# Kernel tuning notes

Hardware: AMD Instinct MI355X
Metric: run time of the kernel (lower is better)

The kernel has to match this reference:

```python
import jax, jax.numpy as jnp
import numpy as np
from jax import lax

B, T, IN, H, OUT = 64, 2048, 128, 256, 1


def setup_inputs() -> dict:
    key = jax.random.key(0)
    ks = jax.random.split(key, 11)
    s_in = 1.0 / np.sqrt(H)
    return {
        "x": jax.random.normal(ks[0], (B, T, IN), dtype=jnp.float32),
        "W_ih0": jax.random.normal(ks[1], (H, IN), dtype=jnp.float32) * s_in,
        "W_hh0": jax.random.normal(ks[2], (H, H), dtype=jnp.float32) * s_in,
        "b_ih0": jax.random.normal(ks[3], (H,), dtype=jnp.float32) * s_in,
        "b_hh0": jax.random.normal(ks[4], (H,), dtype=jnp.float32) * s_in,
        "W_ih1": jax.random.normal(ks[5], (H, H), dtype=jnp.float32) * s_in,
        "W_hh1": jax.random.normal(ks[6], (H, H), dtype=jnp.float32) * s_in,
        "b_ih1": jax.random.normal(ks[7], (H,), dtype=jnp.float32) * s_in,
        "b_hh1": jax.random.normal(ks[8], (H,), dtype=jnp.float32) * s_in,
        "W_fc": jax.random.normal(ks[9], (OUT, H), dtype=jnp.float32) * s_in,
        "b_fc": jax.random.normal(ks[10], (OUT,), dtype=jnp.float32) * s_in,
    }


def _rnn_layer(inp, W_ih, W_hh, b_ih, b_hh):
    # Precompute input projection for all timesteps in one big GEMM: [B,T,H]
    xp = jnp.einsum('bti,hi->bth', inp, W_ih) + b_ih + b_hh
    h0 = jnp.zeros((inp.shape[0], W_hh.shape[0]), dtype=inp.dtype)

    def step(h, xt):  # xt: [B,H]
        h_new = jnp.tanh(xt + h @ W_hh.T)
        return h_new, h_new

    _, hs = lax.scan(step, h0, jnp.swapaxes(xp, 0, 1))  # hs: [T,B,H]
    return jnp.swapaxes(hs, 0, 1)  # [B,T,H]


def reference(x, W_ih0, W_hh0, b_ih0, b_hh0, W_ih1, W_hh1, b_ih1, b_hh1, W_fc, b_fc):
    h1 = _rnn_layer(x, W_ih0, W_hh0, b_ih0, b_hh0)   # layer 0 (dropout_prob=0.0)
    h2 = _rnn_layer(h1, W_ih1, W_hh1, b_ih1, b_hh1)  # layer 1
    last = h2[:, -1, :]                              # [B,H]
    return last @ W_fc.T + b_fc                      # [B,OUT]
```

## Files before the change

### kernel.cpp

```cpp
#include <hip/hip_runtime.h>
#include <math.h>

constexpr int Bb  = 64;
constexpr int Tt  = 2048;
constexpr int INN = 128;
constexpr int HH  = 256;
constexpr int ROWS = Bb * Tt;
constexpr int CH  = 64;
constexpr int NCH = Tt / CH;
constexpr int PS  = HH + 4;

__device__ int g_flag0[Bb];
__device__ int g_flag1[Bb];
__device__ int g_flag1b[Bb];

__device__ __forceinline__ void wait_flag(int* flag, int want)
{
    while (__hip_atomic_load(flag, __ATOMIC_RELAXED,
                             __HIP_MEMORY_SCOPE_SYSTEM) < want)
        __builtin_amdgcn_s_sleep(8);
    __builtin_amdgcn_fence(__ATOMIC_ACQUIRE, "agent");
}

__device__ __forceinline__ void wait_flag2(int* fa, int* fb, int want)
{
    for (;;) {
        int a = __hip_atomic_load(fa, __ATOMIC_RELAXED, __HIP_MEMORY_SCOPE_SYSTEM);
        int c = __hip_atomic_load(fb, __ATOMIC_RELAXED, __HIP_MEMORY_SCOPE_SYSTEM);
        if (a >= want && c >= want) break;
        __builtin_amdgcn_s_sleep(8);
    }
    __builtin_amdgcn_fence(__ATOMIC_ACQUIRE, "agent");
}

__device__ __forceinline__ void release_flag(int* flag, int val)
{
    __hip_atomic_store(flag, val, __ATOMIC_RELEASE, __HIP_MEMORY_SCOPE_AGENT);
}

__device__ __forceinline__ void lds_barrier()
{
    asm volatile("s_waitcnt lgkmcnt(0)" ::: "memory");
    __builtin_amdgcn_s_barrier();
}

__global__ __launch_bounds__(256) void ih_gemm(const float* in, const float* W,
                                               const float* bias1, const float* bias2,
                                               float* out)
{
    __shared__ float a_lds[16][68];
    __shared__ float b_lds[16][260];

    const int tid = threadIdx.x;
    if (blockIdx.x == 0 && tid < Bb) {
        g_flag0[tid] = 0; g_flag1[tid] = 0; g_flag1b[tid] = 0;
    }

    const int tx  = tid & 31;
    const int ty  = tid >> 5;
    const int row0 = blockIdx.x * 64;

    float acc[8][8];
#pragma unroll
    for (int r = 0; r < 8; ++r)
#pragma unroll
        for (int c = 0; c < 8; ++c) acc[r][c] = 0.f;

    for (int k0 = 0; k0 < INN; k0 += 16) {
#pragma unroll
        for (int i = 0; i < 4; ++i) {
            int e = i * 256 + tid;
            int r = e >> 4, kk = e & 15;
            a_lds[kk][r] = in[(row0 + r) * INN + k0 + kk];
        }
#pragma unroll
        for (int i = 0; i < 16; ++i) {
            int e = i * 256 + tid;
            int j = e >> 4, kk = e & 15;
            b_lds[kk][j] = W[j * INN + k0 + kk];
        }
        __syncthreads();

#pragma unroll
        for (int kk = 0; kk < 16; ++kk) {
            float4 a0 = *(const float4*)&a_lds[kk][ty * 8];
            float4 a1 = *(const float4*)&a_lds[kk][ty * 8 + 4];
            float4 b0 = *(const float4*)&b_lds[kk][tx * 8];
            float4 b1 = *(const float4*)&b_lds[kk][tx * 8 + 4];
            float av[8] = {a0.x, a0.y, a0.z, a0.w, a1.x, a1.y, a1.z, a1.w};
            float bv[8] = {b0.x, b0.y, b0.z, b0.w, b1.x, b1.y, b1.z, b1.w};
#pragma unroll
            for (int r = 0; r < 8; ++r)
#pragma unroll
                for (int c = 0; c < 8; ++c)
                    acc[r][c] += av[r] * bv[c];
        }
        __syncthreads();
    }

    float bsum[8];
#pragma unroll
    for (int c = 0; c < 8; ++c) {
        int j = tx * 8 + c;
        bsum[c] = bias1[j] + bias2[j];
    }
#pragma unroll
    for (int r = 0; r < 8; ++r) {
        int row = row0 + ty * 8 + r;
        float4 o0 = make_float4(acc[r][0] + bsum[0], acc[r][1] + bsum[1],
                                acc[r][2] + bsum[2], acc[r][3] + bsum[3]);
        float4 o1 = make_float4(acc[r][4] + bsum[4], acc[r][5] + bsum[5],
                                acc[r][6] + bsum[6], acc[r][7] + bsum[7]);
        *(float4*)&out[row * HH + tx * 8]     = o0;
        *(float4*)&out[row * HH + tx * 8 + 4] = o1;
    }
}

__device__ __forceinline__ float fast_tanh(float x)
{
    float e = __builtin_amdgcn_exp2f(x * 2.8853900817779268f);
    return fmaf(-2.0f, __builtin_amdgcn_rcpf(e + 1.0f), 1.0f);
}

__device__ __forceinline__ float fold32(float s)
{
#if __has_builtin(__builtin_amdgcn_permlane32_swap)
    typedef unsigned uint2v __attribute__((ext_vector_type(2)));
    uint2v r = __builtin_amdgcn_permlane32_swap(__float_as_uint(s), __float_as_uint(s),
                                                false, false);
    return __uint_as_float(r[0]) + __uint_as_float(r[1]);
#else
    return s + __shfl_xor(s, 32, 64);
#endif
}

__device__ __forceinline__ void load_wreg(const float* W, int l, int w,
                                          float (&wreg)[4][32])
{
#pragma unroll
    for (int r = 0; r < 4; ++r) {
        const float4* wp = (const float4*)&W[(size_t)(4 * l + r) * HH + 32 * w];
#pragma unroll
        for (int q = 0; q < 8; ++q) {
            float4 v = wp[q];
            wreg[r][4 * q + 0] = v.x;
            wreg[r][4 * q + 1] = v.y;
            wreg[r][4 * q + 2] = v.z;
            wreg[r][4 * q + 3] = v.w;
        }
    }
}

__device__ __forceinline__ void mac_partials(float hv, const float (&wreg)[4][32],
                                             float* wr)
{
    float p0 = 0.f, p1 = 0.f, p2 = 0.f, p3 = 0.f;
#pragma unroll
    for (int c = 0; c < 32; ++c) {
        float hcv = __int_as_float(__builtin_amdgcn_readlane(__float_as_int(hv), c));
        p0 = fmaf(wreg[0][c], hcv, p0);
        p1 = fmaf(wreg[1][c], hcv, p1);
        p2 = fmaf(wreg[2][c], hcv, p2);
        p3 = fmaf(wreg[3][c], hcv, p3);
    }
    *(float4*)wr = make_float4(p0, p1, p2, p3);
}

template <bool FS>
__device__ __forceinline__ void rnn_step(const float* rd, float* wr,
                                         float*& pw, const float* pr,
                                         float& xg, const float (&wreg)[4][32],
                                         bool lane_lt32)
{
    float xg2 = *pr;

    float s0 = rd[0 * PS], s1 = rd[1 * PS], s2 = rd[2 * PS], s3 = rd[3 * PS];
    float s = (s0 + s1) + (s2 + s3);
    s = fold32(s);

    float hv = fast_tanh(s + xg);
    if (lane_lt32) *pw = hv;

    mac_partials(hv, wreg, wr);

    if (FS) __syncthreads(); else lds_barrier();
    xg = xg2;
    pw += HH;
}

template <bool PROD>
__device__ void rnn_role(float* xpb, const float* Whh, float* sh, int b)
{
    float* pbufA = sh;
    float* pbufB = sh + 8 * PS;

    const int tid = threadIdx.x;
    const int w   = tid >> 6;
    const int l   = tid & 63;
    const int hf  = l >> 5;
    const int jr  = 32 * w + (l & 31);
    const bool lane_lt32 = (l < 32);

    float wreg[4][32];
    load_wreg(Whh, l, w, wreg);

    const float* rdA = &pbufA[4 * hf * PS + jr];
    const float* rdB = &pbufB[4 * hf * PS + jr];
    float*       wrA = &pbufA[w * PS + 4 * l];
    float*       wrB = &pbufB[w * PS + 4 * l];

    *(float4*)wrA = make_float4(0.f, 0.f, 0.f, 0.f);
    float xg = PROD ? xpb[jr] : 0.f;
    float* pw = xpb + jr;
    const float* pr = xpb + HH + jr;
    __syncthreads();

#pragma unroll 1
    for (int c = 0; c < NCH; ++c) {
        if (!PROD) {
            wait_flag2(&g_flag1[b], &g_flag1b[b], (c + 1) * (CH / 2));
            xg = xpb[(size_t)c * CH * HH + jr];
        }
#pragma unroll 1
        for (int p = 0; p < CH / 2 - 1; ++p) {
            rnn_step<false>(rdA, wrB, pw, pr, xg, wreg, lane_lt32); pr += HH;
            rnn_step<false>(rdB, wrA, pw, pr, xg, wreg, lane_lt32); pr += HH;
        }
        if (c < NCH - 1) {
            rnn_step<false>(rdA, wrB, pw, pr, xg, wreg, lane_lt32); pr += HH;
            rnn_step<PROD>(rdB, wrA, pw, pr, xg, wreg, lane_lt32);  pr += HH;
        } else {
            rnn_step<false>(rdA, wrB, pw, pr, xg, wreg, lane_lt32);
            rnn_step<PROD>(rdB, wrA, pw, pr, xg, wreg, lane_lt32);
        }
        if (PROD && tid == 0)
            release_flag(&g_flag0[b], (c + 1) * CH);
    }
}

__device__ __forceinline__ void gemm_phase(const float* rd, float* wr,
                                           float*& pw, const float* pr,
                                           float& xg, const float (&wreg)[4][32],
                                           float bsc, bool lane_lt32)
{
    float xg2 = *pr;

    float s0 = rd[0 * PS], s1 = rd[1 * PS], s2 = rd[2 * PS], s3 = rd[3 * PS];
    float s = (s0 + s1) + (s2 + s3);
    s = fold32(s);
    if (lane_lt32) *pw = s + bsc;

    mac_partials(xg, wreg, wr);

    lds_barrier();
    xg = xg2;
    pw += HH;
}

__device__ void gemm_role(float* ws, const float* W,
                          const float* b1, const float* b2, float* sh,
                          int b, int half)
{
    float* pbufA = sh;
    float* pbufB = sh + 8 * PS;

    const int tid = threadIdx.x;
    const int w   = tid >> 6;
    const int l   = tid & 63;
    const int hf  = l >> 5;
    const int jr  = 32 * w + (l & 31);
    const bool lane_lt32 = (l < 32);

    float wreg[4][32];
    load_wreg(W, l, w, wreg);
    const float bsc = b1[jr] + b2[jr];

    const float* rdA = &pbufA[4 * hf * PS + jr];
    const float* rdB = &pbufB[4 * hf * PS + jr];
    float*       wrA = &pbufA[w * PS + 4 * l];
    float*       wrB = &pbufB[w * PS + 4 * l];

    int* myflag = half ? &g_flag1b[b] : &g_flag1[b];

#pragma unroll 1
    for (int c = 0; c < NCH; ++c) {
        wait_flag(&g_flag0[b], (c + 1) * CH);

        float* Ab = ws + ((size_t)b * Tt + (size_t)c * CH + 32 * half) * HH;

        float xg  = Ab[jr];
        float xg2 = Ab[HH + jr];
        mac_partials(xg, wreg, wrB);
        lds_barrier();
        xg = xg2;

        float* pw = Ab + jr;
        const float* pr = Ab + 2 * HH + jr;

#pragma unroll 1
        for (int p = 0; p < 15; ++p) {
            gemm_phase(rdB, wrA, pw, pr, xg, wreg, bsc, lane_lt32); pr += HH;
            gemm_phase(rdA, wrB, pw, pr, xg, wreg, bsc, lane_lt32); pr += HH;
        }
        gemm_phase(rdB, wrA, pw, pr - HH, xg, wreg, bsc, lane_lt32);

        {
            float s0 = rdA[0 * PS], s1 = rdA[1 * PS];
            float s2 = rdA[2 * PS], s3 = rdA[3 * PS];
            float s = (s0 + s1) + (s2 + s3);
            s = fold32(s);
            if (lane_lt32) *pw = s + bsc;
            __syncthreads();
        }

        if (tid == 0)
            release_flag(myflag, (c + 1) * (CH / 2));
    }
}

__global__ __launch_bounds__(512, 2) void pipeline_kernel(
        float* ws, const float* Whh0, const float* Wih1,
        const float* bih1, const float* bhh1, const float* Whh1)
{
    __shared__ __attribute__((aligned(16))) float sh[2 * 8 * PS];

    const int bid = blockIdx.x;

    if (bid < 64) {
        rnn_role<true>(ws + (size_t)bid * Tt * HH, Whh0, sh, bid);
    } else if (bid < 192) {
        const int pidx = bid - 64;
        gemm_role(ws, Wih1, bih1, bhh1, sh, pidx >> 1, pidx & 1);
    } else {
        const int b = bid - 192;
        rnn_role<false>(ws + (size_t)b * Tt * HH, Whh1, sh, b);
    }
}

__global__ __launch_bounds__(64) void fc_kernel(const float* h2, const float* Wfc,
                                                const float* bfc, float* out)
{
    const int b = blockIdx.x;
    const int l = threadIdx.x;
    const float* hrow = h2 + ((size_t)b * Tt + (Tt - 1)) * HH;
    float4 hv = *(const float4*)&hrow[4 * l];
    float4 wv = *(const float4*)&Wfc[4 * l];
    float p = hv.x * wv.x + hv.y * wv.y + hv.z * wv.z + hv.w * wv.w;
#pragma unroll
    for (int off = 32; off > 0; off >>= 1) p += __shfl_down(p, off, 64);
    if (l == 0) out[b] = p + bfc[0];
}

extern "C" void kernel_launch(void* const* d_in, const int* in_sizes, int n_in,
                              void* d_out, int out_size, void* d_ws, size_t ws_size,
                              hipStream_t stream)
{
    const float* x     = (const float*)d_in[0];
    const float* W_ih0 = (const float*)d_in[1];
    const float* W_hh0 = (const float*)d_in[2];
    const float* b_ih0 = (const float*)d_in[3];
    const float* b_hh0 = (const float*)d_in[4];
    const float* W_ih1 = (const float*)d_in[5];
    const float* W_hh1 = (const float*)d_in[6];
    const float* b_ih1 = (const float*)d_in[7];
    const float* b_hh1 = (const float*)d_in[8];
    const float* W_fc  = (const float*)d_in[9];
    const float* b_fc  = (const float*)d_in[10];
    float* ws  = (float*)d_ws;
    float* out = (float*)d_out;

    ih_gemm<<<ROWS / 64, 256, 0, stream>>>(x, W_ih0, b_ih0, b_hh0, ws);
    pipeline_kernel<<<256, 512, 0, stream>>>(ws, W_hh0, W_ih1, b_ih1, b_hh1, W_hh1);
    fc_kernel<<<Bb, 64, 0, stream>>>(ws, W_fc, b_fc, out);
}
```

Measured before the change: 1.509 ms.

## Use packed f32x2 FMAs in matvec and deepen input prefetch to two steps

Stores the recurrent weight registers as float2 vectors so the per-step 32-term matvec can compile to packed FMA instructions, which halves the FMA instruction count at the cost of a final horizontal add. It also prefetches the input projection two steps ahead instead of one, so global load latency is hidden across more of the serial recurrence. The gemm loop is restructured with clamped read pointers to keep the prefetch in bounds. Register pressure rises slightly from the extra prefetch, and summation order changes.

```diff
diff --git a/kernel.cpp b/kernel.cpp
--- a/kernel.cpp
+++ b/kernel.cpp
@@ -10,6 +10,8 @@
 constexpr int NCH = Tt / CH;
 constexpr int PS  = HH + 4;
 
+typedef float f32x2 __attribute__((ext_vector_type(2)));
+
 __device__ int g_flag0[Bb];
 __device__ int g_flag1[Bb];
 __device__ int g_flag1b[Bb];
@@ -135,44 +137,42 @@
 }
 
 __device__ __forceinline__ void load_wreg(const float* W, int l, int w,
-                                          float (&wreg)[4][32])
+                                          f32x2 (&wreg)[4][16])
 {
 #pragma unroll
     for (int r = 0; r < 4; ++r) {
-        const float4* wp = (const float4*)&W[(size_t)(4 * l + r) * HH + 32 * w];
-#pragma unroll
-        for (int q = 0; q < 8; ++q) {
-            float4 v = wp[q];
-            wreg[r][4 * q + 0] = v.x;
-            wreg[r][4 * q + 1] = v.y;
-            wreg[r][4 * q + 2] = v.z;
-            wreg[r][4 * q + 3] = v.w;
-        }
-    }
-}
-
-__device__ __forceinline__ void mac_partials(float hv, const float (&wreg)[4][32],
+        const f32x2* wp = (const f32x2*)&W[(size_t)(4 * l + r) * HH + 32 * w];
+#pragma unroll
+        for (int c = 0; c < 16; ++c) wreg[r][c] = wp[c];
+    }
+}
+
+__device__ __forceinline__ void mac_partials(float hv, const f32x2 (&wreg)[4][16],
                                              float* wr)
 {
-    float p0 = 0.f, p1 = 0.f, p2 = 0.f, p3 = 0.f;
-#pragma unroll
-    for (int c = 0; c < 32; ++c) {
-        float hcv = __int_as_float(__builtin_amdgcn_readlane(__float_as_int(hv), c));
-        p0 = fmaf(wreg[0][c], hcv, p0);
-        p1 = fmaf(wreg[1][c], hcv, p1);
-        p2 = fmaf(wreg[2][c], hcv, p2);
-        p3 = fmaf(wreg[3][c], hcv, p3);
-    }
-    *(float4*)wr = make_float4(p0, p1, p2, p3);
+    f32x2 a0 = {0.f, 0.f}, a1 = {0.f, 0.f}, a2 = {0.f, 0.f}, a3 = {0.f, 0.f};
+#pragma unroll
+    for (int c = 0; c < 16; ++c) {
+        f32x2 h2;
+        h2.x = __int_as_float(__builtin_amdgcn_readlane(__float_as_int(hv), 2 * c));
+        h2.y = __int_as_float(__builtin_amdgcn_readlane(__float_as_int(hv), 2 * c + 1));
+        a0 += wreg[0][c] * h2;
+        a1 += wreg[1][c] * h2;
+        a2 += wreg[2][c] * h2;
+        a3 += wreg[3][c] * h2;
+    }
+    *(float4*)wr = make_float4(a0.x + a0.y, a1.x + a1.y,
+                               a2.x + a2.y, a3.x + a3.y);
 }
 
 template <bool FS>
 __device__ __forceinline__ void rnn_step(const float* rd, float* wr,
                                          float*& pw, const float* pr,
-                                         float& xg, const float (&wreg)[4][32],
+                                         float& xg, float& xgn,
+                                         const f32x2 (&wreg)[4][16],
                                          bool lane_lt32)
 {
-    float xg2 = *pr;
+    float xg3 = *pr;
 
     float s0 = rd[0 * PS], s1 = rd[1 * PS], s2 = rd[2 * PS], s3 = rd[3 * PS];
     float s = (s0 + s1) + (s2 + s3);
@@ -184,7 +184,7 @@
     mac_partials(hv, wreg, wr);
 
     if (FS) __syncthreads(); else lds_barrier();
-    xg = xg2;
+    xg = xgn; xgn = xg3;
     pw += HH;
 }
 
@@ -201,7 +201,7 @@
     const int jr  = 32 * w + (l & 31);
     const bool lane_lt32 = (l < 32);
 
-    float wreg[4][32];
+    f32x2 wreg[4][16];
     load_wreg(Whh, l, w, wreg);
 
     const float* rdA = &pbufA[4 * hf * PS + jr];
@@ -210,28 +210,36 @@
     float*       wrB = &pbufB[w * PS + 4 * l];
 
     *(float4*)wrA = make_float4(0.f, 0.f, 0.f, 0.f);
-    float xg = PROD ? xpb[jr] : 0.f;
+    float xg  = PROD ? xpb[jr] : 0.f;
+    float xgn = PROD ? xpb[HH + jr] : 0.f;
     float* pw = xpb + jr;
-    const float* pr = xpb + HH + jr;
+    const float* pr = xpb + 2 * HH + jr;
     __syncthreads();
 
 #pragma unroll 1
     for (int c = 0; c < NCH; ++c) {
         if (!PROD) {
             wait_flag2(&g_flag1[b], &g_flag1b[b], (c + 1) * (CH / 2));
-            xg = xpb[(size_t)c * CH * HH + jr];
-        }
-#pragma unroll 1
-        for (int p = 0; p < CH / 2 - 1; ++p) {
-            rnn_step<false>(rdA, wrB, pw, pr, xg, wreg, lane_lt32); pr += HH;
-            rnn_step<false>(rdB, wrA, pw, pr, xg, wreg, lane_lt32); pr += HH;
+            const float* rb = xpb + (size_t)c * CH * HH + jr;
+            xg = rb[0]; xgn = rb[HH];
         }
         if (c < NCH - 1) {
-            rnn_step<false>(rdA, wrB, pw, pr, xg, wreg, lane_lt32); pr += HH;
-            rnn_step<PROD>(rdB, wrA, pw, pr, xg, wreg, lane_lt32);  pr += HH;
+#pragma unroll 1
+            for (int p = 0; p < CH / 2 - 1; ++p) {
+                rnn_step<false>(rdA, wrB, pw, pr, xg, xgn, wreg, lane_lt32); pr += HH;
+                rnn_step<false>(rdB, wrA, pw, pr, xg, xgn, wreg, lane_lt32); pr += HH;
+            }
+            rnn_step<false>(rdA, wrB, pw, pr, xg, xgn, wreg, lane_lt32); pr += HH;
+            rnn_step<PROD>(rdB, wrA, pw, pr, xg, xgn, wreg, lane_lt32);  pr += HH;
         } else {
-            rnn_step<false>(rdA, wrB, pw, pr, xg, wreg, lane_lt32);
-            rnn_step<PROD>(rdB, wrA, pw, pr, xg, wreg, lane_lt32);
+#pragma unroll 1
+            for (int p = 0; p < CH / 2 - 1; ++p) {
+                rnn_step<false>(rdA, wrB, pw, pr, xg, xgn, wreg, lane_lt32); pr += HH;
+                rnn_step<false>(rdB, wrA, pw, pr, xg, xgn, wreg, lane_lt32); pr += HH;
+            }
+            const float* prc = xpb + (size_t)(Tt - 1) * HH + jr;
+            rnn_step<false>(rdA, wrB, pw, prc, xg, xgn, wreg, lane_lt32);
+            rnn_step<PROD>(rdB, wrA, pw, prc, xg, xgn, wreg, lane_lt32);
         }
         if (PROD && tid == 0)
             release_flag(&g_flag0[b], (c + 1) * CH);
@@ -240,10 +248,11 @@
 
 __device__ __forceinline__ void gemm_phase(const float* rd, float* wr,
                                            float*& pw, const float* pr,
-                                           float& xg, const float (&wreg)[4][32],
+                                           float& xg, float& xgn,
+                                           const f32x2 (&wreg)[4][16],
                                            float bsc, bool lane_lt32)
 {
-    float xg2 = *pr;
+    float xg3 = *pr;
 
     float s0 = rd[0 * PS], s1 = rd[1 * PS], s2 = rd[2 * PS], s3 = rd[3 * PS];
     float s = (s0 + s1) + (s2 + s3);
@@ -253,7 +262,7 @@
     mac_partials(xg, wreg, wr);
 
     lds_barrier();
-    xg = xg2;
+    xg = xgn; xgn = xg3;
     pw += HH;
 }
 
@@ -271,7 +280,7 @@
     const int jr  = 32 * w + (l & 31);
     const bool lane_lt32 = (l < 32);
 
-    float wreg[4][32];
+    f32x2 wreg[4][16];
     load_wreg(W, l, w, wreg);
     const float bsc = b1[jr] + b2[jr];
 
@@ -289,20 +298,25 @@
         float* Ab = ws + ((size_t)b * Tt + (size_t)c * CH + 32 * half) * HH;
 
         float xg  = Ab[jr];
-        float xg2 = Ab[HH + jr];
-        mac_partials(xg, wreg, wrB);
-        lds_barrier();
-        xg = xg2;
+        float xgn = Ab[HH + jr];
+        const float* pr = Ab + 2 * HH + jr;
+        const float* prclamp = Ab + 31 * HH + jr;
+        {
+            float xg3 = *pr; pr += HH;
+            mac_partials(xg, wreg, wrB);
+            lds_barrier();
+            xg = xgn; xgn = xg3;
+        }
 
         float* pw = Ab + jr;
-        const float* pr = Ab + 2 * HH + jr;
-
-#pragma unroll 1
-        for (int p = 0; p < 15; ++p) {
-            gemm_phase(rdB, wrA, pw, pr, xg, wreg, bsc, lane_lt32); pr += HH;
-            gemm_phase(rdA, wrB, pw, pr, xg, wreg, bsc, lane_lt32); pr += HH;
-        }
-        gemm_phase(rdB, wrA, pw, pr - HH, xg, wreg, bsc, lane_lt32);
+
+#pragma unroll 1
+        for (int p = 1; p < 32; ++p) {
+            const float* prc = (p <= 29) ? pr : prclamp;
+            if (p & 1) gemm_phase(rdB, wrA, pw, prc, xg, xgn, wreg, bsc, lane_lt32);
+            else       gemm_phase(rdA, wrB, pw, prc, xg, xgn, wreg, bsc, lane_lt32);
+            pr += HH;
+        }
 
         {
             float s0 = rdA[0 * PS], s1 = rdA[1 * PS];
```

After: 1.608 ms. +6.5%, slower.

## Deepen xproj prefetch to two steps, skip layer-1 h stores, shorten spin sleep

Applied to the files above, without the earlier changes.

Global loads of the input projection now run two steps ahead (xg/xgn rotation) instead of one in both the recurrent and GEMM roles. This hides more global-memory latency behind the serial per-step chain. The layer-1 consumer no longer writes every hidden state back to global memory and stores only the final step. Flag spin-waits sleep for a shorter interval to cut wake-up latency. In exchange, the GEMM loop gets a per-iteration branch and clamped pointers, and polling traffic on the flags goes up.

```diff
diff --git a/kernel.cpp b/kernel.cpp
--- a/kernel.cpp
+++ b/kernel.cpp
@@ -18,7 +18,7 @@
 {
     while (__hip_atomic_load(flag, __ATOMIC_RELAXED,
                              __HIP_MEMORY_SCOPE_SYSTEM) < want)
-        __builtin_amdgcn_s_sleep(8);
+        __builtin_amdgcn_s_sleep(2);
     __builtin_amdgcn_fence(__ATOMIC_ACQUIRE, "agent");
 }
 
@@ -28,7 +28,7 @@
         int a = __hip_atomic_load(fa, __ATOMIC_RELAXED, __HIP_MEMORY_SCOPE_SYSTEM);
         int c = __hip_atomic_load(fb, __ATOMIC_RELAXED, __HIP_MEMORY_SCOPE_SYSTEM);
         if (a >= want && c >= want) break;
-        __builtin_amdgcn_s_sleep(8);
+        __builtin_amdgcn_s_sleep(2);
     }
     __builtin_amdgcn_fence(__ATOMIC_ACQUIRE, "agent");
 }
@@ -169,22 +169,23 @@
 template <bool FS>
 __device__ __forceinline__ void rnn_step(const float* rd, float* wr,
                                          float*& pw, const float* pr,
-                                         float& xg, const float (&wreg)[4][32],
-                                         bool lane_lt32)
-{
-    float xg2 = *pr;
+                                         float& xg, float& xgn,
+                                         const float (&wreg)[4][32],
+                                         bool lane_lt32, bool store_h)
+{
+    float xg3 = *pr;
 
     float s0 = rd[0 * PS], s1 = rd[1 * PS], s2 = rd[2 * PS], s3 = rd[3 * PS];
     float s = (s0 + s1) + (s2 + s3);
     s = fold32(s);
 
     float hv = fast_tanh(s + xg);
-    if (lane_lt32) *pw = hv;
+    if (store_h && lane_lt32) *pw = hv;
 
     mac_partials(hv, wreg, wr);
 
     if (FS) __syncthreads(); else lds_barrier();
-    xg = xg2;
+    xg = xgn; xgn = xg3;
     pw += HH;
 }
 
@@ -210,28 +211,36 @@
     float*       wrB = &pbufB[w * PS + 4 * l];
 
     *(float4*)wrA = make_float4(0.f, 0.f, 0.f, 0.f);
-    float xg = PROD ? xpb[jr] : 0.f;
+    float xg  = PROD ? xpb[jr] : 0.f;
+    float xgn = PROD ? xpb[HH + jr] : 0.f;
     float* pw = xpb + jr;
-    const float* pr = xpb + HH + jr;
+    const float* pr = xpb + 2 * HH + jr;
     __syncthreads();
 
 #pragma unroll 1
     for (int c = 0; c < NCH; ++c) {
         if (!PROD) {
             wait_flag2(&g_flag1[b], &g_flag1b[b], (c + 1) * (CH / 2));
-            xg = xpb[(size_t)c * CH * HH + jr];
-        }
-#pragma unroll 1
-        for (int p = 0; p < CH / 2 - 1; ++p) {
-            rnn_step<false>(rdA, wrB, pw, pr, xg, wreg, lane_lt32); pr += HH;
-            rnn_step<false>(rdB, wrA, pw, pr, xg, wreg, lane_lt32); pr += HH;
+            const float* rb = xpb + (size_t)c * CH * HH + jr;
+            xg = rb[0]; xgn = rb[HH];
         }
         if (c < NCH - 1) {
-            rnn_step<false>(rdA, wrB, pw, pr, xg, wreg, lane_lt32); pr += HH;
-            rnn_step<PROD>(rdB, wrA, pw, pr, xg, wreg, lane_lt32);  pr += HH;
+#pragma unroll 1
+            for (int p = 0; p < CH / 2 - 1; ++p) {
+                rnn_step<false>(rdA, wrB, pw, pr, xg, xgn, wreg, lane_lt32, PROD); pr += HH;
+                rnn_step<false>(rdB, wrA, pw, pr, xg, xgn, wreg, lane_lt32, PROD); pr += HH;
+            }
+            rnn_step<false>(rdA, wrB, pw, pr, xg, xgn, wreg, lane_lt32, PROD); pr += HH;
+            rnn_step<PROD>(rdB, wrA, pw, pr, xg, xgn, wreg, lane_lt32, PROD);  pr += HH;
         } else {
-            rnn_step<false>(rdA, wrB, pw, pr, xg, wreg, lane_lt32);
-            rnn_step<PROD>(rdB, wrA, pw, pr, xg, wreg, lane_lt32);
+#pragma unroll 1
+            for (int p = 0; p < CH / 2 - 1; ++p) {
+                rnn_step<false>(rdA, wrB, pw, pr, xg, xgn, wreg, lane_lt32, PROD); pr += HH;
+                rnn_step<false>(rdB, wrA, pw, pr, xg, xgn, wreg, lane_lt32, PROD); pr += HH;
+            }
+            const float* prc = xpb + (size_t)(Tt - 1) * HH + jr;
+            rnn_step<false>(rdA, wrB, pw, prc, xg, xgn, wreg, lane_lt32, PROD);
+            rnn_step<PROD>(rdB, wrA, pw, prc, xg, xgn, wreg, lane_lt32, true);
         }
         if (PROD && tid == 0)
             release_flag(&g_flag0[b], (c + 1) * CH);
@@ -240,10 +249,11 @@
 
 __device__ __forceinline__ void gemm_phase(const float* rd, float* wr,
                                            float*& pw, const float* pr,
-                                           float& xg, const float (&wreg)[4][32],
+                                           float& xg, float& xgn,
+                                           const float (&wreg)[4][32],
                                            float bsc, bool lane_lt32)
 {
-    float xg2 = *pr;
+    float xg3 = *pr;
 
     float s0 = rd[0 * PS], s1 = rd[1 * PS], s2 = rd[2 * PS], s3 = rd[3 * PS];
     float s = (s0 + s1) + (s2 + s3);
@@ -253,7 +263,7 @@
     mac_partials(xg, wreg, wr);
 
     lds_barrier();
-    xg = xg2;
+    xg = xgn; xgn = xg3;
     pw += HH;
 }
 
@@ -289,20 +299,25 @@
         float* Ab = ws + ((size_t)b * Tt + (size_t)c * CH + 32 * half) * HH;
 
         float xg  = Ab[jr];
-        float xg2 = Ab[HH + jr];
-        mac_partials(xg, wreg, wrB);
-        lds_barrier();
-        xg = xg2;
+        float xgn = Ab[HH + jr];
+        const float* pr = Ab + 2 * HH + jr;
+        const float* prclamp = Ab + 31 * HH + jr;
+        {
+            float xg3 = *pr; pr += HH;
+            mac_partials(xg, wreg, wrB);
+            lds_barrier();
+            xg = xgn; xgn = xg3;
+        }
 
         float* pw = Ab + jr;
-        const float* pr = Ab + 2 * HH + jr;
-
-#pragma unroll 1
-        for (int p = 0; p < 15; ++p) {
-            gemm_phase(rdB, wrA, pw, pr, xg, wreg, bsc, lane_lt32); pr += HH;
-            gemm_phase(rdA, wrB, pw, pr, xg, wreg, bsc, lane_lt32); pr += HH;
-        }
-        gemm_phase(rdB, wrA, pw, pr - HH, xg, wreg, bsc, lane_lt32);
+
+#pragma unroll 1
+        for (int p = 1; p < 32; ++p) {
+            const float* prc = (p <= 29) ? pr : prclamp;
+            if (p & 1) gemm_phase(rdB, wrA, pw, prc, xg, xgn, wreg, bsc, lane_lt32);
+            else       gemm_phase(rdA, wrB, pw, prc, xg, xgn, wreg, bsc, lane_lt32);
+            pr += HH;
+        }
 
         {
             float s0 = rdA[0 * PS], s1 = rdA[1 * PS];
```

New measurement: 1.435 ms, median of 2. -4.9%, faster.
